# Kernel tuning notes

Hardware: AMD Instinct MI355X
Metric: run time of the kernel (lower is better)

The kernel has to match this reference:

```python
import jax, jax.numpy as jnp
import numpy as np

B, T, SDR, D, H = 2, 1024, 2048, 1024, 16
DH = D // H
FFN_H = int(D * 4.0 * 2 / 3)  # SwiGLU 2/3 rule -> 2730
N_FHN_STEPS = 4
FHN_DT = 0.1
FHN_A = 0.7
FHN_B = 0.8
FHN_TAU = 12.5
FHN_THRESHOLD = 0.5


def _layernorm(x, g, b, eps=1e-5):
    mu = jnp.mean(x, axis=-1, keepdims=True)
    var = jnp.var(x, axis=-1, keepdims=True)
    return (x - mu) * jax.lax.rsqrt(var + eps) * g + b


def setup_inputs() -> dict:
    key = jax.random.key(0)
    ks = jax.random.split(key, 16)
    s = 0.02
    return {
        "sdr": jax.random.normal(ks[0], (B, T, SDR), jnp.float32),
        "sdr_w": jax.random.normal(ks[1], (SDR, D), jnp.float32) * s,
        "sdr_b": jnp.zeros((D,), jnp.float32),
        "w_qkv": jax.random.normal(ks[2], (D, 3 * D), jnp.float32) * s,
        "b_qkv": jnp.zeros((3 * D,), jnp.float32),
        "w_out": jax.random.normal(ks[3], (D, D), jnp.float32) * s,
        "b_out": jnp.zeros((D,), jnp.float32),
        "ln1_g": jnp.ones((D,), jnp.float32),
        "ln1_b": jnp.zeros((D,), jnp.float32),
        "ln2_g": jnp.ones((D,), jnp.float32),
        "ln2_b": jnp.zeros((D,), jnp.float32),
        "w_gate": jax.random.normal(ks[4], (D, FFN_H), jnp.float32) * s,
        "w_up": jax.random.normal(ks[5], (D, FFN_H), jnp.float32) * s,
        "w_down": jax.random.normal(ks[6], (FFN_H, D), jnp.float32) * s,
    }


def _fhn_attention(h, w_qkv, b_qkv, w_out, b_out):
    # h: (B, T, D). Causal MHA whose pre-softmax scores are evolved by
    # FitzHugh-Nagumo soliton dynamics with IMEX (explicit v, implicit w) steps.
    qkv = h @ w_qkv + b_qkv
    q, k, vals = jnp.split(qkv, 3, axis=-1)
    q = q.reshape(B, T, H, DH).transpose(0, 2, 1, 3)      # bhtd
    k = k.reshape(B, T, H, DH).transpose(0, 2, 1, 3)
    vals = vals.reshape(B, T, H, DH).transpose(0, 2, 1, 3)
    scores = jnp.einsum("bhqd,bhkd->bhqk", q, k) / jnp.sqrt(jnp.float32(DH))
    # FHN IMEX integration: v' = v - v^3/3 - w + I ; tau w' = v + a - b w
    v = scores
    w = jnp.zeros_like(scores)
    w_denom = 1.0 + FHN_DT * FHN_B / FHN_TAU
    for _ in range(N_FHN_STEPS):
        v = v + FHN_DT * (v - v * v * v / 3.0 - w + scores)  # explicit
        w = (w + FHN_DT * (v + FHN_A) / FHN_TAU) / w_denom   # implicit linear
    logits = v - FHN_THRESHOLD
    causal = jnp.tril(jnp.ones((T, T), bool))
    logits = jnp.where(causal, logits, -1e9)
    attn = jax.nn.softmax(logits, axis=-1)
    ctx = jnp.einsum("bhqk,bhkd->bhqd", attn, vals)
    ctx = ctx.transpose(0, 2, 1, 3).reshape(B, T, D)
    return ctx @ w_out + b_out


def reference(sdr, sdr_w, sdr_b, w_qkv, b_qkv, w_out, b_out,
              ln1_g, ln1_b, ln2_g, ln2_b, w_gate, w_up, w_down):
    x = sdr @ sdr_w + sdr_b                                   # sdr_proj
    attn_out = _fhn_attention(_layernorm(x, ln1_g, ln1_b),
                              w_qkv, b_qkv, w_out, b_out)
    x = x + attn_out                                          # residual
    h2 = _layernorm(x, ln2_g, ln2_b)
    mlp = (jax.nn.silu(h2 @ w_gate) * (h2 @ w_up)) @ w_down   # SwiGLU
    return x + mlp
```

## Files before the change

kernel.cpp:

```cpp
#include <hip/hip_runtime.h>
#include <hip/hip_bf16.h>
#include <math.h>


typedef __bf16 bf16;
typedef __bf16 bf16x4 __attribute__((ext_vector_type(4)));
typedef __bf16 bf16x8 __attribute__((ext_vector_type(8)));
typedef float  f32x4  __attribute__((ext_vector_type(4)));

#define DEV __device__ __forceinline__

DEV void gload_lds16(const void* g, void* l) {
  __builtin_amdgcn_global_load_lds(
      (const __attribute__((address_space(1))) void*)g,
      (__attribute__((address_space(3))) void*)l, 16, 0, 0);
}

__global__ __launch_bounds__(256) void k_convert(const float* __restrict__ in,
                                                 bf16* __restrict__ out, int n) {
  int i = (blockIdx.x * 256 + threadIdx.x) * 4;
  if (i < n) {
    float4 f = *(const float4*)(in + i);
    bf16x4 o;
    o[0] = (bf16)f.x; o[1] = (bf16)f.y; o[2] = (bf16)f.z; o[3] = (bf16)f.w;
    *(bf16x4*)(out + i) = o;
  }
}

__global__ __launch_bounds__(256) void k_transpose_wt(const float* __restrict__ in,
    bf16* __restrict__ out, int K, int N, int Kpad, int Npad) {
  __shared__ float tile[32][33];
  const int kb = blockIdx.x * 32, nb = blockIdx.y * 32;
  const int tx = threadIdx.x & 31, ty = threadIdx.x >> 5;
  for (int i = ty; i < 32; i += 8) {
    int k = kb + i, n = nb + tx;
    tile[i][tx] = (k < K && n < N) ? in[(size_t)k * N + n] : 0.f;
  }
  __syncthreads();
  for (int i = ty; i < 32; i += 8) {
    int n = nb + i, k = kb + tx;
    if (n < Npad && k < Kpad) out[(size_t)n * Kpad + k] = (bf16)tile[tx][i];
  }
}

__global__ __launch_bounds__(256) void k_layernorm(const float* __restrict__ x,
    const float* __restrict__ gw, const float* __restrict__ bw, bf16* __restrict__ out) {
  const int row = blockIdx.x;
  const int t = threadIdx.x;
  const float* xr = x + (size_t)row * 1024;
  float4 f = *(const float4*)(xr + t * 4);
  float s  = f.x + f.y + f.z + f.w;
  float s2 = f.x * f.x + f.y * f.y + f.z * f.z + f.w * f.w;
  #pragma unroll
  for (int o = 32; o > 0; o >>= 1) { s += __shfl_down(s, o, 64); s2 += __shfl_down(s2, o, 64); }
  __shared__ float rA[4], rB[4];
  const int wid = t >> 6;
  if ((t & 63) == 0) { rA[wid] = s; rB[wid] = s2; }
  __syncthreads();
  s  = rA[0] + rA[1] + rA[2] + rA[3];
  s2 = rB[0] + rB[1] + rB[2] + rB[3];
  const float mu   = s * (1.f / 1024.f);
  const float var  = fmaxf(s2 * (1.f / 1024.f) - mu * mu, 0.f);
  const float rstd = rsqrtf(var + 1e-5f);
  float4 g4 = *(const float4*)(gw + t * 4);
  float4 b4 = *(const float4*)(bw + t * 4);
  bf16x4 o4;
  o4[0] = (bf16)((f.x - mu) * rstd * g4.x + b4.x);
  o4[1] = (bf16)((f.y - mu) * rstd * g4.y + b4.y);
  o4[2] = (bf16)((f.z - mu) * rstd * g4.z + b4.z);
  o4[3] = (bf16)((f.w - mu) * rstd * g4.w + b4.w);
  *(bf16x4*)(out + (size_t)row * 1024 + t * 4) = o4;
}

enum { EPI_BIAS = 1, EPI_BIAS_RES = 2, EPI_RES = 3, EPI_QKV = 5 };

template <int EPI>
DEV void gemm_epilogue(int rb, int cc, int Nn, const f32x4& a,
                       float* C, const float* bias, const float* res,
                       bf16* qp, bf16* kp, float* vbuf) {
  float bv = 0.f;
  if constexpr (EPI == EPI_BIAS || EPI == EPI_BIAS_RES || EPI == EPI_QKV) bv = bias[cc];
  #pragma unroll
  for (int v = 0; v < 4; ++v) {
    const int row = rb + v;
    float val = a[v] + bv;
    if constexpr (EPI == EPI_QKV) {
      const int bq = row >> 10, tt = row & 1023;
      if (cc < 1024) {
        qp[(size_t)(bq * 16 + (cc >> 6)) * 65536 + (size_t)tt * 64 + (cc & 63)] = (bf16)(val * 0.125f);
      } else if (cc < 2048) {
        const int c2 = cc - 1024;
        kp[(size_t)(bq * 16 + (c2 >> 6)) * 65536 + (size_t)tt * 64 + (c2 & 63)] = (bf16)val;
      } else {
        vbuf[(size_t)row * 1024 + (cc - 2048)] = val;
      }
    } else {
      const size_t idx = (size_t)row * Nn + cc;
      if constexpr (EPI == EPI_BIAS_RES || EPI == EPI_RES) val += res[idx];
      C[idx] = val;
    }
  }
}

template <int EPI>
__global__ __launch_bounds__(256, 2)
void k_gemm(const bf16* __restrict__ A, const bf16* __restrict__ Bt,
            float* __restrict__ C, const float* __restrict__ bias,
            const float* __restrict__ res, bf16* __restrict__ qp,
            bf16* __restrict__ kp, float* __restrict__ vbuf, int Nn, int Kk) {
  __shared__ __align__(16) bf16 As[128 * 64];
  __shared__ __align__(16) bf16 Bs[128 * 64];
  const int t = threadIdx.x;
  const int lane = t & 63, wid = t >> 6;
  const int wr = wid >> 1, wc = wid & 1;
  const int row0 = blockIdx.y * 128, col0 = blockIdx.x * 128;
  const int g  = t & 7;
  const int r0 = t >> 3;
  const int c16s = g ^ (r0 & 7);
  f32x4 acc[4][4] = {};

  for (int k0 = 0; k0 < Kk; k0 += 64) {
    #pragma unroll
    for (int it = 0; it < 4; ++it) {
      int r = r0 + it * 32;
      gload_lds16(A + (size_t)(row0 + r) * Kk + k0 + c16s * 8, &As[(it * 256 + wid * 64) * 8]);
    }
    #pragma unroll
    for (int it = 0; it < 4; ++it) {
      int r = r0 + it * 32;
      gload_lds16(Bt + (size_t)(col0 + r) * Kk + k0 + c16s * 8, &Bs[(it * 256 + wid * 64) * 8]);
    }
    __syncthreads();
    #pragma unroll
    for (int ks = 0; ks < 2; ++ks) {
      bf16x8 af[4], bfv[4];
      #pragma unroll
      for (int m = 0; m < 4; ++m) {
        int rr = wr * 64 + m * 16 + (lane & 15);
        int c16 = (ks * 4 + (lane >> 4)) ^ (rr & 7);
        af[m] = *(const bf16x8*)&As[rr * 64 + c16 * 8];
      }
      #pragma unroll
      for (int n = 0; n < 4; ++n) {
        int rr = wc * 64 + n * 16 + (lane & 15);
        int c16 = (ks * 4 + (lane >> 4)) ^ (rr & 7);
        bfv[n] = *(const bf16x8*)&Bs[rr * 64 + c16 * 8];
      }
      #pragma unroll
      for (int m = 0; m < 4; ++m)
        #pragma unroll
        for (int n = 0; n < 4; ++n)
          acc[m][n] = __builtin_amdgcn_mfma_f32_16x16x32_bf16(af[m], bfv[n], acc[m][n], 0, 0, 0);
    }
    __syncthreads();
  }
  #pragma unroll
  for (int m = 0; m < 4; ++m) {
    const int rb = row0 + wr * 64 + m * 16 + ((lane >> 4) << 2);
    #pragma unroll
    for (int n = 0; n < 4; ++n) {
      const int cc = col0 + wc * 64 + n * 16 + (lane & 15);
      gemm_epilogue<EPI>(rb, cc, Nn, acc[m][n], C, bias, res, qp, kp, vbuf);
    }
  }
}

template <int EPI>
__global__ __launch_bounds__(256, 2)
void k_gemm64(const bf16* __restrict__ A, const bf16* __restrict__ Bt,
              float* __restrict__ C, const float* __restrict__ bias,
              const float* __restrict__ res, int Nn, int Kk) {
  __shared__ __align__(16) bf16 As[128 * 64];
  __shared__ __align__(16) bf16 Bs[64 * 64];
  const int t = threadIdx.x;
  const int lane = t & 63, wid = t >> 6;
  const int row0 = blockIdx.y * 128, col0 = blockIdx.x * 64;
  const int g  = t & 7;
  const int r0 = t >> 3;
  const int c16s = g ^ (r0 & 7);
  f32x4 acc[2][4] = {};

  for (int k0 = 0; k0 < Kk; k0 += 64) {
    #pragma unroll
    for (int it = 0; it < 4; ++it) {
      int r = r0 + it * 32;
      gload_lds16(A + (size_t)(row0 + r) * Kk + k0 + c16s * 8, &As[(it * 256 + wid * 64) * 8]);
    }
    #pragma unroll
    for (int it = 0; it < 2; ++it) {
      int r = r0 + it * 32;
      gload_lds16(Bt + (size_t)(col0 + r) * Kk + k0 + c16s * 8, &Bs[(it * 256 + wid * 64) * 8]);
    }
    __syncthreads();
    #pragma unroll
    for (int ks = 0; ks < 2; ++ks) {
      bf16x8 af[2], bfv[4];
      #pragma unroll
      for (int m = 0; m < 2; ++m) {
        int rr = wid * 32 + m * 16 + (lane & 15);
        int c16 = (ks * 4 + (lane >> 4)) ^ (rr & 7);
        af[m] = *(const bf16x8*)&As[rr * 64 + c16 * 8];
      }
      #pragma unroll
      for (int n = 0; n < 4; ++n) {
        int rr = n * 16 + (lane & 15);
        int c16 = (ks * 4 + (lane >> 4)) ^ (rr & 7);
        bfv[n] = *(const bf16x8*)&Bs[rr * 64 + c16 * 8];
      }
      #pragma unroll
      for (int m = 0; m < 2; ++m)
        #pragma unroll
        for (int n = 0; n < 4; ++n)
          acc[m][n] = __builtin_amdgcn_mfma_f32_16x16x32_bf16(af[m], bfv[n], acc[m][n], 0, 0, 0);
    }
    __syncthreads();
  }
  #pragma unroll
  for (int m = 0; m < 2; ++m) {
    const int rb = row0 + wid * 32 + m * 16 + ((lane >> 4) << 2);
    #pragma unroll
    for (int n = 0; n < 4; ++n) {
      const int cc = col0 + n * 16 + (lane & 15);
      gemm_epilogue<EPI>(rb, cc, Nn, acc[m][n], C, bias, res, nullptr, nullptr, nullptr);
    }
  }
}

__global__ __launch_bounds__(256, 2)
void k_gemm_swiglu(const bf16* __restrict__ A, const bf16* __restrict__ Bg,
                   const bf16* __restrict__ Bu, bf16* __restrict__ act,
                   int Nn, int Kk) {
  __shared__ __align__(16) bf16 As[128 * 64];
  __shared__ __align__(16) bf16 Bgs[128 * 64];
  __shared__ __align__(16) bf16 Bus[128 * 64];
  const int t = threadIdx.x;
  const int lane = t & 63, wid = t >> 6;
  const int wr = wid >> 1, wc = wid & 1;
  const int row0 = blockIdx.y * 128, col0 = blockIdx.x * 128;
  const int g  = t & 7;
  const int r0 = t >> 3;
  const int c16s = g ^ (r0 & 7);
  f32x4 ag[4][4] = {}, au[4][4] = {};

  for (int k0 = 0; k0 < Kk; k0 += 64) {
    #pragma unroll
    for (int it = 0; it < 4; ++it) {
      int r = r0 + it * 32;
      gload_lds16(A + (size_t)(row0 + r) * Kk + k0 + c16s * 8, &As[(it * 256 + wid * 64) * 8]);
    }
    #pragma unroll
    for (int it = 0; it < 4; ++it) {
      int r = r0 + it * 32;
      gload_lds16(Bg + (size_t)(col0 + r) * Kk + k0 + c16s * 8, &Bgs[(it * 256 + wid * 64) * 8]);
    }
    #pragma unroll
    for (int it = 0; it < 4; ++it) {
      int r = r0 + it * 32;
      gload_lds16(Bu + (size_t)(col0 + r) * Kk + k0 + c16s * 8, &Bus[(it * 256 + wid * 64) * 8]);
    }
    __syncthreads();
    #pragma unroll
    for (int ks = 0; ks < 2; ++ks) {
      bf16x8 af[4], bg[4], bu[4];
      #pragma unroll
      for (int m = 0; m < 4; ++m) {
        int rr = wr * 64 + m * 16 + (lane & 15);
        int c16 = (ks * 4 + (lane >> 4)) ^ (rr & 7);
        af[m] = *(const bf16x8*)&As[rr * 64 + c16 * 8];
      }
      #pragma unroll
      for (int n = 0; n < 4; ++n) {
        int rr = wc * 64 + n * 16 + (lane & 15);
        int c16 = (ks * 4 + (lane >> 4)) ^ (rr & 7);
        bg[n] = *(const bf16x8*)&Bgs[rr * 64 + c16 * 8];
        bu[n] = *(const bf16x8*)&Bus[rr * 64 + c16 * 8];
      }
      #pragma unroll
      for (int m = 0; m < 4; ++m)
        #pragma unroll
        for (int n = 0; n < 4; ++n) {
          ag[m][n] = __builtin_amdgcn_mfma_f32_16x16x32_bf16(af[m], bg[n], ag[m][n], 0, 0, 0);
          au[m][n] = __builtin_amdgcn_mfma_f32_16x16x32_bf16(af[m], bu[n], au[m][n], 0, 0, 0);
        }
    }
    __syncthreads();
  }
  #pragma unroll
  for (int m = 0; m < 4; ++m) {
    const int rb = row0 + wr * 64 + m * 16 + ((lane >> 4) << 2);
    #pragma unroll
    for (int n = 0; n < 4; ++n) {
      const int cc = col0 + wc * 64 + n * 16 + (lane & 15);
      #pragma unroll
      for (int v = 0; v < 4; ++v) {
        float gt = ag[m][n][v], up = au[m][n][v];
        float sg = gt / (1.f + __expf(-gt));
        act[(size_t)(rb + v) * Nn + cc] = (bf16)(sg * up);
      }
    }
  }
}

__global__ __launch_bounds__(256) void k_transpose_v(const float* __restrict__ vbuf,
                                                     bf16* __restrict__ vT) {
  __shared__ float tile[32][33];
  const int bh = blockIdx.z, b = bh >> 4, h = bh & 15;
  const int t0 = blockIdx.x * 32, d0 = blockIdx.y * 32;
  const int tx = threadIdx.x & 31, ty = threadIdx.x >> 5;
  for (int i = ty; i < 32; i += 8)
    tile[i][tx] = vbuf[(size_t)(b * 1024 + t0 + i) * 1024 + h * 64 + d0 + tx];
  __syncthreads();
  for (int i = ty; i < 32; i += 8)
    vT[(size_t)bh * 65536 + (size_t)(d0 + i) * 1024 + t0 + tx] = (bf16)tile[tx][i];
}

#define FHN_DT 0.1f
#define FHN_A_ 0.7f

__global__ __launch_bounds__(256, 4)
void k_attn(const bf16* __restrict__ q, const bf16* __restrict__ k,
            const bf16* __restrict__ vT, bf16* __restrict__ ctx) {
  __shared__ __align__(16) char smem[16896];
  const int bx = blockIdx.x;
  const int s  = 63 - (bx >> 5);
  const int bh = bx & 31;
  const int b = bh >> 4, hh = bh & 15;
  const int t = threadIdx.x;
  const int lane = t & 63, wid = t >> 6;
  const int l15 = lane & 15, g4 = lane >> 4;
  const int q0 = s * 16;
  bf16* Ps    = (bf16*)smem + wid * 1024;
  float* comb = (float*)smem;
  float* mlb  = (float*)(smem + 16384);
  const bf16* qb = q  + (size_t)bh * 65536;
  const bf16* kb = k  + (size_t)bh * 65536;
  const bf16* vb = vT + (size_t)bh * 65536;
  const float wden = 1.0f / (1.0f + FHN_DT * 0.8f / 12.5f);
  const float dtau = FHN_DT / 12.5f;

  bf16x8 qf[2];
  #pragma unroll
  for (int ks = 0; ks < 2; ++ks)
    qf[ks] = *(const bf16x8*)(qb + (size_t)(q0 + l15) * 64 + ks * 32 + g4 * 8);

  f32x4 o[4] = {};
  f32x4 mrow = {-1e30f, -1e30f, -1e30f, -1e30f};
  f32x4 ssum = {0.f, 0.f, 0.f, 0.f};
  const int jn = (q0 >> 6) + 1;

  for (int j = wid; j < jn; j += 4) {
    const int kv0 = j * 64;
    f32x4 sc[4] = {};
    #pragma unroll
    for (int ks = 0; ks < 2; ++ks)
      #pragma unroll
      for (int n = 0; n < 4; ++n) {
        bf16x8 kf = *(const bf16x8*)(kb + (size_t)(kv0 + n * 16 + l15) * 64 + ks * 32 + g4 * 8);
        sc[n] = __builtin_amdgcn_mfma_f32_16x16x32_bf16(qf[ks], kf, sc[n], 0, 0, 0);
      }
    const int rbase = q0 + (g4 << 2);
    #pragma unroll
    for (int n = 0; n < 4; ++n)
      #pragma unroll
      for (int v = 0; v < 4; ++v) {
        float sv = sc[n][v];
        float vv = sv, ww = 0.f;
        #pragma unroll
        for (int st = 0; st < 4; ++st) {
          vv = vv + FHN_DT * (vv - vv * vv * vv * (1.f / 3.f) - ww + sv);
          ww = (ww + dtau * (vv + FHN_A_)) * wden;
        }
        float lg = vv - 0.5f;
        if (j == jn - 1) {
          int kvi = kv0 + n * 16 + l15;
          if (kvi > rbase + v) lg = -1e9f;
        }
        sc[n][v] = lg;
      }
    f32x4 mnew, scl;
    #pragma unroll
    for (int v = 0; v < 4; ++v) {
      float m0 = fmaxf(fmaxf(sc[0][v], sc[1][v]), fmaxf(sc[2][v], sc[3][v]));
      #pragma unroll
      for (int msk = 1; msk < 16; msk <<= 1) m0 = fmaxf(m0, __shfl_xor(m0, msk, 64));
      mnew[v] = fmaxf(mrow[v], m0);
      scl[v] = __expf(mrow[v] - mnew[v]);
    }
    #pragma unroll
    for (int v = 0; v < 4; ++v) {
      float rs = 0.f;
      #pragma unroll
      for (int n = 0; n < 4; ++n) {
        float p = __expf(sc[n][v] - mnew[v]);
        sc[n][v] = p;
        rs += p;
      }
      #pragma unroll
      for (int msk = 1; msk < 16; msk <<= 1) rs += __shfl_xor(rs, msk, 64);
      ssum[v] = ssum[v] * scl[v] + rs;
      mrow[v] = mnew[v];
    }
    #pragma unroll
    for (int n = 0; n < 4; ++n) o[n] *= scl;
    #pragma unroll
    for (int n = 0; n < 4; ++n)
      #pragma unroll
      for (int v = 0; v < 4; ++v) {
        int rr = (g4 << 2) + v;
        int c = n * 16 + l15;
        int c16 = (c >> 3) ^ (rr & 7);
        Ps[rr * 64 + c16 * 8 + (c & 7)] = (bf16)sc[n][v];
      }
    #pragma unroll
    for (int ks = 0; ks < 2; ++ks) {
      int c16 = (ks * 4 + g4) ^ (l15 & 7);
      bf16x8 pa = *(const bf16x8*)&Ps[l15 * 64 + c16 * 8];
      #pragma unroll
      for (int n = 0; n < 4; ++n) {
        bf16x8 vf = *(const bf16x8*)(vb + (size_t)(n * 16 + l15) * 1024 + kv0 + ks * 32 + g4 * 8);
        o[n] = __builtin_amdgcn_mfma_f32_16x16x32_bf16(pa, vf, o[n], 0, 0, 0);
      }
    }
  }
  __syncthreads();
  #pragma unroll
  for (int n = 0; n < 4; ++n)
    #pragma unroll
    for (int v = 0; v < 4; ++v)
      comb[(wid * 16 + (g4 << 2) + v) * 64 + n * 16 + l15] = o[n][v];
  if (l15 == 0) {
    #pragma unroll
    for (int v = 0; v < 4; ++v) {
      mlb[(wid * 16 + (g4 << 2) + v) * 2 + 0] = mrow[v];
      mlb[(wid * 16 + (g4 << 2) + v) * 2 + 1] = ssum[v];
    }
  }
  __syncthreads();
  {
    const int row = t >> 4, dseg = t & 15;
    float m = mlb[row * 2];
    #pragma unroll
    for (int w = 1; w < 4; ++w) m = fmaxf(m, mlb[(w * 16 + row) * 2]);
    float L = 0.f;
    f32x4 a = {0.f, 0.f, 0.f, 0.f};
    #pragma unroll
    for (int w = 0; w < 4; ++w) {
      float f = __expf(mlb[(w * 16 + row) * 2] - m);
      L += f * mlb[(w * 16 + row) * 2 + 1];
      f32x4 c = *(const f32x4*)&comb[(w * 16 + row) * 64 + dseg * 4];
      a += c * f;
    }
    const float inv = 1.f / L;
    bf16x4 o4;
    o4[0] = (bf16)(a[0] * inv); o4[1] = (bf16)(a[1] * inv);
    o4[2] = (bf16)(a[2] * inv); o4[3] = (bf16)(a[3] * inv);
    *(bf16x4*)&ctx[(size_t)(b * 1024 + q0 + row) * 1024 + hh * 64 + dseg * 4] = o4;
  }
}

extern "C" void kernel_launch(void* const* d_in, const int* in_sizes, int n_in,
                              void* d_out, int out_size, void* d_ws, size_t ws_size,
                              hipStream_t stream) {
  (void)in_sizes; (void)n_in; (void)out_size; (void)ws_size;
  const float* sdr    = (const float*)d_in[0];
  const float* sdr_w  = (const float*)d_in[1];
  const float* sdr_b  = (const float*)d_in[2];
  const float* w_qkv  = (const float*)d_in[3];
  const float* b_qkv  = (const float*)d_in[4];
  const float* w_out  = (const float*)d_in[5];
  const float* b_out  = (const float*)d_in[6];
  const float* ln1_g  = (const float*)d_in[7];
  const float* ln1_b  = (const float*)d_in[8];
  const float* ln2_g  = (const float*)d_in[9];
  const float* ln2_b  = (const float*)d_in[10];
  const float* w_gate = (const float*)d_in[11];
  const float* w_up   = (const float*)d_in[12];
  const float* w_down = (const float*)d_in[13];
  float* out = (float*)d_out;

  char* wsb = (char*)d_ws;
  size_t off = 0;
  auto alloc = [&](size_t bytes) -> void* {
    void* p = (void*)(wsb + off);
    off += (bytes + 255) & ~(size_t)255;
    return p;
  };
  bf16* sdr_w_t  = (bf16*)alloc(1024ull * 2048 * 2);
  bf16* w_qkv_t  = (bf16*)alloc(3072ull * 1024 * 2);
  bf16* w_out_t  = (bf16*)alloc(1024ull * 1024 * 2);
  bf16* w_gate_t = (bf16*)alloc(2816ull * 1024 * 2);
  bf16* w_up_t   = (bf16*)alloc(2816ull * 1024 * 2);
  bf16* w_down_t = (bf16*)alloc(1024ull * 2816 * 2);
  bf16* big_bf   = (bf16*)alloc(2048ull * 2816 * 2);
  bf16* sdr_bf   = big_bf;
  bf16* act      = big_bf;
  float* x       = (float*)alloc(2048ull * 1024 * 4);
  bf16*  h       = (bf16*)alloc(2048ull * 1024 * 2);
  float* vbuf    = (float*)alloc(2048ull * 1024 * 4);
  bf16*  qb      = (bf16*)alloc(32ull * 1024 * 64 * 2);
  bf16*  kb      = (bf16*)alloc(32ull * 1024 * 64 * 2);
  bf16*  vT      = (bf16*)alloc(32ull * 1024 * 64 * 2);
  bf16*  ctx     = (bf16*)alloc(2048ull * 1024 * 2);
  float* x2      = (float*)alloc(2048ull * 1024 * 4);

  k_convert<<<4096, 256, 0, stream>>>(sdr, sdr_bf, 4194304);
  k_transpose_wt<<<dim3(64, 32),  256, 0, stream>>>(sdr_w,  sdr_w_t,  2048, 1024, 2048, 1024);
  k_transpose_wt<<<dim3(32, 96),  256, 0, stream>>>(w_qkv,  w_qkv_t,  1024, 3072, 1024, 3072);
  k_transpose_wt<<<dim3(32, 32),  256, 0, stream>>>(w_out,  w_out_t,  1024, 1024, 1024, 1024);
  k_transpose_wt<<<dim3(32, 88),  256, 0, stream>>>(w_gate, w_gate_t, 1024, 2730, 1024, 2816);
  k_transpose_wt<<<dim3(32, 88),  256, 0, stream>>>(w_up,   w_up_t,   1024, 2730, 1024, 2816);
  k_transpose_wt<<<dim3(88, 32),  256, 0, stream>>>(w_down, w_down_t, 2730, 1024, 2816, 1024);

  k_gemm64<EPI_BIAS><<<dim3(16, 16), 256, 0, stream>>>(sdr_bf, sdr_w_t, x, sdr_b, nullptr, 1024, 2048);
  k_layernorm<<<2048, 256, 0, stream>>>(x, ln1_g, ln1_b, h);
  k_gemm<EPI_QKV><<<dim3(24, 16), 256, 0, stream>>>(h, w_qkv_t, nullptr, b_qkv, nullptr, qb, kb, vbuf, 3072, 1024);
  k_transpose_v<<<dim3(32, 2, 32), 256, 0, stream>>>(vbuf, vT);
  k_attn<<<2048, 256, 0, stream>>>(qb, kb, vT, ctx);
  k_gemm64<EPI_BIAS_RES><<<dim3(16, 16), 256, 0, stream>>>(ctx, w_out_t, x2, b_out, x, 1024, 1024);
  k_layernorm<<<2048, 256, 0, stream>>>(x2, ln2_g, ln2_b, h);
  k_gemm_swiglu<<<dim3(22, 16), 256, 0, stream>>>(h, w_gate_t, w_up_t, act, 2816, 1024);
  k_gemm64<EPI_RES><<<dim3(16, 16), 256, 0, stream>>>(act, w_down_t, out, nullptr, x2, 1024, 2816);
}
```

Measured before the change: 356.6 us.

## Double-buffer GEMM LDS tiles and pair causal attention query blocks per workgroup

The k_gemm and k_gemm64 kernels now keep two LDS buffers, so the next K-slice's global-to-LDS loads are issued before the MFMA work on the current slice. This is meant to hide load latency, and it doubles the shared memory used per block, which may lower occupancy. The attention kernel now runs two query tiles per block, a long one (63-pr) and a short one (pr), and launches half as many blocks. This balances the causal workload across blocks and cuts scheduling overhead.

```diff
diff --git a/kernel.cpp b/kernel.cpp
--- a/kernel.cpp
+++ b/kernel.cpp
@@ -108,8 +108,8 @@
             float* __restrict__ C, const float* __restrict__ bias,
             const float* __restrict__ res, bf16* __restrict__ qp,
             bf16* __restrict__ kp, float* __restrict__ vbuf, int Nn, int Kk) {
-  __shared__ __align__(16) bf16 As[128 * 64];
-  __shared__ __align__(16) bf16 Bs[128 * 64];
+  __shared__ __align__(16) bf16 As[2][128 * 64];
+  __shared__ __align__(16) bf16 Bs[2][128 * 64];
   const int t = threadIdx.x;
   const int lane = t & 63, wid = t >> 6;
   const int wr = wid >> 1, wc = wid & 1;
@@ -119,18 +119,24 @@
   const int c16s = g ^ (r0 & 7);
   f32x4 acc[4][4] = {};
 
+  auto stage = [&](int buf, int k0) {
+    #pragma unroll
+    for (int it = 0; it < 4; ++it) {
+      int r = r0 + it * 32;
+      gload_lds16(A + (size_t)(row0 + r) * Kk + k0 + c16s * 8, &As[buf][(it * 256 + wid * 64) * 8]);
+    }
+    #pragma unroll
+    for (int it = 0; it < 4; ++it) {
+      int r = r0 + it * 32;
+      gload_lds16(Bt + (size_t)(col0 + r) * Kk + k0 + c16s * 8, &Bs[buf][(it * 256 + wid * 64) * 8]);
+    }
+  };
+
+  stage(0, 0);
+  __syncthreads();
+  int cur = 0;
   for (int k0 = 0; k0 < Kk; k0 += 64) {
-    #pragma unroll
-    for (int it = 0; it < 4; ++it) {
-      int r = r0 + it * 32;
-      gload_lds16(A + (size_t)(row0 + r) * Kk + k0 + c16s * 8, &As[(it * 256 + wid * 64) * 8]);
-    }
-    #pragma unroll
-    for (int it = 0; it < 4; ++it) {
-      int r = r0 + it * 32;
-      gload_lds16(Bt + (size_t)(col0 + r) * Kk + k0 + c16s * 8, &Bs[(it * 256 + wid * 64) * 8]);
-    }
-    __syncthreads();
+    if (k0 + 64 < Kk) stage(cur ^ 1, k0 + 64);
     #pragma unroll
     for (int ks = 0; ks < 2; ++ks) {
       bf16x8 af[4], bfv[4];
@@ -138,13 +144,13 @@
       for (int m = 0; m < 4; ++m) {
         int rr = wr * 64 + m * 16 + (lane & 15);
         int c16 = (ks * 4 + (lane >> 4)) ^ (rr & 7);
-        af[m] = *(const bf16x8*)&As[rr * 64 + c16 * 8];
+        af[m] = *(const bf16x8*)&As[cur][rr * 64 + c16 * 8];
       }
       #pragma unroll
       for (int n = 0; n < 4; ++n) {
         int rr = wc * 64 + n * 16 + (lane & 15);
         int c16 = (ks * 4 + (lane >> 4)) ^ (rr & 7);
-        bfv[n] = *(const bf16x8*)&Bs[rr * 64 + c16 * 8];
+        bfv[n] = *(const bf16x8*)&Bs[cur][rr * 64 + c16 * 8];
       }
       #pragma unroll
       for (int m = 0; m < 4; ++m)
@@ -153,6 +159,7 @@
           acc[m][n] = __builtin_amdgcn_mfma_f32_16x16x32_bf16(af[m], bfv[n], acc[m][n], 0, 0, 0);
     }
     __syncthreads();
+    cur ^= 1;
   }
   #pragma unroll
   for (int m = 0; m < 4; ++m) {
@@ -170,8 +177,8 @@
 void k_gemm64(const bf16* __restrict__ A, const bf16* __restrict__ Bt,
               float* __restrict__ C, const float* __restrict__ bias,
               const float* __restrict__ res, int Nn, int Kk) {
-  __shared__ __align__(16) bf16 As[128 * 64];
-  __shared__ __align__(16) bf16 Bs[64 * 64];
+  __shared__ __align__(16) bf16 As[2][128 * 64];
+  __shared__ __align__(16) bf16 Bs[2][64 * 64];
   const int t = threadIdx.x;
   const int lane = t & 63, wid = t >> 6;
   const int row0 = blockIdx.y * 128, col0 = blockIdx.x * 64;
@@ -180,18 +187,24 @@
   const int c16s = g ^ (r0 & 7);
   f32x4 acc[2][4] = {};
 
+  auto stage = [&](int buf, int k0) {
+    #pragma unroll
+    for (int it = 0; it < 4; ++it) {
+      int r = r0 + it * 32;
+      gload_lds16(A + (size_t)(row0 + r) * Kk + k0 + c16s * 8, &As[buf][(it * 256 + wid * 64) * 8]);
+    }
+    #pragma unroll
+    for (int it = 0; it < 2; ++it) {
+      int r = r0 + it * 32;
+      gload_lds16(Bt + (size_t)(col0 + r) * Kk + k0 + c16s * 8, &Bs[buf][(it * 256 + wid * 64) * 8]);
+    }
+  };
+
+  stage(0, 0);
+  __syncthreads();
+  int cur = 0;
   for (int k0 = 0; k0 < Kk; k0 += 64) {
-    #pragma unroll
-    for (int it = 0; it < 4; ++it) {
-      int r = r0 + it * 32;
-      gload_lds16(A + (size_t)(row0 + r) * Kk + k0 + c16s * 8, &As[(it * 256 + wid * 64) * 8]);
-    }
-    #pragma unroll
-    for (int it = 0; it < 2; ++it) {
-      int r = r0 + it * 32;
-      gload_lds16(Bt + (size_t)(col0 + r) * Kk + k0 + c16s * 8, &Bs[(it * 256 + wid * 64) * 8]);
-    }
-    __syncthreads();
+    if (k0 + 64 < Kk) stage(cur ^ 1, k0 + 64);
     #pragma unroll
     for (int ks = 0; ks < 2; ++ks) {
       bf16x8 af[2], bfv[4];
@@ -199,13 +212,13 @@
       for (int m = 0; m < 2; ++m) {
         int rr = wid * 32 + m * 16 + (lane & 15);
         int c16 = (ks * 4 + (lane >> 4)) ^ (rr & 7);
-        af[m] = *(const bf16x8*)&As[rr * 64 + c16 * 8];
+        af[m] = *(const bf16x8*)&As[cur][rr * 64 + c16 * 8];
       }
       #pragma unroll
       for (int n = 0; n < 4; ++n) {
         int rr = n * 16 + (lane & 15);
         int c16 = (ks * 4 + (lane >> 4)) ^ (rr & 7);
-        bfv[n] = *(const bf16x8*)&Bs[rr * 64 + c16 * 8];
+        bfv[n] = *(const bf16x8*)&Bs[cur][rr * 64 + c16 * 8];
       }
       #pragma unroll
       for (int m = 0; m < 2; ++m)
@@ -214,6 +227,7 @@
           acc[m][n] = __builtin_amdgcn_mfma_f32_16x16x32_bf16(af[m], bfv[n], acc[m][n], 0, 0, 0);
     }
     __syncthreads();
+    cur ^= 1;
   }
   #pragma unroll
   for (int m = 0; m < 2; ++m) {
@@ -322,13 +336,12 @@
             const bf16* __restrict__ vT, bf16* __restrict__ ctx) {
   __shared__ __align__(16) char smem[16896];
   const int bx = blockIdx.x;
-  const int s  = 63 - (bx >> 5);
+  const int pr = bx >> 5;
   const int bh = bx & 31;
   const int b = bh >> 4, hh = bh & 15;
   const int t = threadIdx.x;
   const int lane = t & 63, wid = t >> 6;
   const int l15 = lane & 15, g4 = lane >> 4;
-  const int q0 = s * 16;
   bf16* Ps    = (bf16*)smem + wid * 1024;
   float* comb = (float*)smem;
   float* mlb  = (float*)(smem + 16384);
@@ -338,123 +351,129 @@
   const float wden = 1.0f / (1.0f + FHN_DT * 0.8f / 12.5f);
   const float dtau = FHN_DT / 12.5f;
 
-  bf16x8 qf[2];
-  #pragma unroll
-  for (int ks = 0; ks < 2; ++ks)
-    qf[ks] = *(const bf16x8*)(qb + (size_t)(q0 + l15) * 64 + ks * 32 + g4 * 8);
-
-  f32x4 o[4] = {};
-  f32x4 mrow = {-1e30f, -1e30f, -1e30f, -1e30f};
-  f32x4 ssum = {0.f, 0.f, 0.f, 0.f};
-  const int jn = (q0 >> 6) + 1;
-
-  for (int j = wid; j < jn; j += 4) {
-    const int kv0 = j * 64;
-    f32x4 sc[4] = {};
+  #pragma unroll 1
+  for (int ph = 0; ph < 2; ++ph) {
+    const int s  = ph ? pr : 63 - pr;
+    const int q0 = s * 16;
+    bf16x8 qf[2];
     #pragma unroll
     for (int ks = 0; ks < 2; ++ks)
-      #pragma unroll
-      for (int n = 0; n < 4; ++n) {
-        bf16x8 kf = *(const bf16x8*)(kb + (size_t)(kv0 + n * 16 + l15) * 64 + ks * 32 + g4 * 8);
-        sc[n] = __builtin_amdgcn_mfma_f32_16x16x32_bf16(qf[ks], kf, sc[n], 0, 0, 0);
-      }
-    const int rbase = q0 + (g4 << 2);
+      qf[ks] = *(const bf16x8*)(qb + (size_t)(q0 + l15) * 64 + ks * 32 + g4 * 8);
+
+    f32x4 o[4] = {};
+    f32x4 mrow = {-1e30f, -1e30f, -1e30f, -1e30f};
+    f32x4 ssum = {0.f, 0.f, 0.f, 0.f};
+    const int jn = (q0 >> 6) + 1;
+
+    for (int j = wid; j < jn; j += 4) {
+      const int kv0 = j * 64;
+      f32x4 sc[4] = {};
+      #pragma unroll
+      for (int ks = 0; ks < 2; ++ks)
+        #pragma unroll
+        for (int n = 0; n < 4; ++n) {
+          bf16x8 kf = *(const bf16x8*)(kb + (size_t)(kv0 + n * 16 + l15) * 64 + ks * 32 + g4 * 8);
+          sc[n] = __builtin_amdgcn_mfma_f32_16x16x32_bf16(qf[ks], kf, sc[n], 0, 0, 0);
+        }
+      const int rbase = q0 + (g4 << 2);
+      #pragma unroll
+      for (int n = 0; n < 4; ++n)
+        #pragma unroll
+        for (int v = 0; v < 4; ++v) {
+          float sv = sc[n][v];
+          float vv = sv, ww = 0.f;
+          #pragma unroll
+          for (int st = 0; st < 4; ++st) {
+            vv = vv + FHN_DT * (vv - vv * vv * vv * (1.f / 3.f) - ww + sv);
+            ww = (ww + dtau * (vv + FHN_A_)) * wden;
+          }
+          float lg = vv - 0.5f;
+          if (j == jn - 1) {
+            int kvi = kv0 + n * 16 + l15;
+            if (kvi > rbase + v) lg = -1e9f;
+          }
+          sc[n][v] = lg;
+        }
+      f32x4 mnew, scl;
+      #pragma unroll
+      for (int v = 0; v < 4; ++v) {
+        float m0 = fmaxf(fmaxf(sc[0][v], sc[1][v]), fmaxf(sc[2][v], sc[3][v]));
+        #pragma unroll
+        for (int msk = 1; msk < 16; msk <<= 1) m0 = fmaxf(m0, __shfl_xor(m0, msk, 64));
+        mnew[v] = fmaxf(mrow[v], m0);
+        scl[v] = __expf(mrow[v] - mnew[v]);
+      }
+      #pragma unroll
+      for (int v = 0; v < 4; ++v) {
+        float rs = 0.f;
+        #pragma unroll
+        for (int n = 0; n < 4; ++n) {
+          float p = __expf(sc[n][v] - mnew[v]);
+          sc[n][v] = p;
+          rs += p;
+        }
+        #pragma unroll
+        for (int msk = 1; msk < 16; msk <<= 1) rs += __shfl_xor(rs, msk, 64);
+        ssum[v] = ssum[v] * scl[v] + rs;
+        mrow[v] = mnew[v];
+      }
+      #pragma unroll
+      for (int n = 0; n < 4; ++n) o[n] *= scl;
+      #pragma unroll
+      for (int n = 0; n < 4; ++n)
+        #pragma unroll
+        for (int v = 0; v < 4; ++v) {
+          int rr = (g4 << 2) + v;
+          int c = n * 16 + l15;
+          int c16 = (c >> 3) ^ (rr & 7);
+          Ps[rr * 64 + c16 * 8 + (c & 7)] = (bf16)sc[n][v];
+        }
+      #pragma unroll
+      for (int ks = 0; ks < 2; ++ks) {
+        int c16 = (ks * 4 + g4) ^ (l15 & 7);
+        bf16x8 pa = *(const bf16x8*)&Ps[l15 * 64 + c16 * 8];
+        #pragma unroll
+        for (int n = 0; n < 4; ++n) {
+          bf16x8 vf = *(const bf16x8*)(vb + (size_t)(n * 16 + l15) * 1024 + kv0 + ks * 32 + g4 * 8);
+          o[n] = __builtin_amdgcn_mfma_f32_16x16x32_bf16(pa, vf, o[n], 0, 0, 0);
+        }
+      }
+    }
+    __syncthreads();
     #pragma unroll
     for (int n = 0; n < 4; ++n)
       #pragma unroll
+      for (int v = 0; v < 4; ++v)
+        comb[(wid * 16 + (g4 << 2) + v) * 64 + n * 16 + l15] = o[n][v];
+    if (l15 == 0) {
+      #pragma unroll
       for (int v = 0; v < 4; ++v) {
-        float sv = sc[n][v];
-        float vv = sv, ww = 0.f;
-        #pragma unroll
-        for (int st = 0; st < 4; ++st) {
-          vv = vv + FHN_DT * (vv - vv * vv * vv * (1.f / 3.f) - ww + sv);
-          ww = (ww + dtau * (vv + FHN_A_)) * wden;
-        }
-        float lg = vv - 0.5f;
-        if (j == jn - 1) {
-          int kvi = kv0 + n * 16 + l15;
-          if (kvi > rbase + v) lg = -1e9f;
-        }
-        sc[n][v] = lg;
-      }
-    f32x4 mnew, scl;
-    #pragma unroll
-    for (int v = 0; v < 4; ++v) {
-      float m0 = fmaxf(fmaxf(sc[0][v], sc[1][v]), fmaxf(sc[2][v], sc[3][v]));
-      #pragma unroll
-      for (int msk = 1; msk < 16; msk <<= 1) m0 = fmaxf(m0, __shfl_xor(m0, msk, 64));
-      mnew[v] = fmaxf(mrow[v], m0);
-      scl[v] = __expf(mrow[v] - mnew[v]);
-    }
-    #pragma unroll
-    for (int v = 0; v < 4; ++v) {
-      float rs = 0.f;
-      #pragma unroll
-      for (int n = 0; n < 4; ++n) {
-        float p = __expf(sc[n][v] - mnew[v]);
-        sc[n][v] = p;
-        rs += p;
-      }
-      #pragma unroll
-      for (int msk = 1; msk < 16; msk <<= 1) rs += __shfl_xor(rs, msk, 64);
-      ssum[v] = ssum[v] * scl[v] + rs;
-      mrow[v] = mnew[v];
-    }
-    #pragma unroll
-    for (int n = 0; n < 4; ++n) o[n] *= scl;
-    #pragma unroll
-    for (int n = 0; n < 4; ++n)
-      #pragma unroll
-      for (int v = 0; v < 4; ++v) {
-        int rr = (g4 << 2) + v;
-        int c = n * 16 + l15;
-        int c16 = (c >> 3) ^ (rr & 7);
-        Ps[rr * 64 + c16 * 8 + (c & 7)] = (bf16)sc[n][v];
-      }
-    #pragma unroll
-    for (int ks = 0; ks < 2; ++ks) {
-      int c16 = (ks * 4 + g4) ^ (l15 & 7);
-      bf16x8 pa = *(const bf16x8*)&Ps[l15 * 64 + c16 * 8];
-      #pragma unroll
-      for (int n = 0; n < 4; ++n) {
-        bf16x8 vf = *(const bf16x8*)(vb + (size_t)(n * 16 + l15) * 1024 + kv0 + ks * 32 + g4 * 8);
-        o[n] = __builtin_amdgcn_mfma_f32_16x16x32_bf16(pa, vf, o[n], 0, 0, 0);
-      }
-    }
-  }
-  __syncthreads();
-  #pragma unroll
-  for (int n = 0; n < 4; ++n)
-    #pragma unroll
-    for (int v = 0; v < 4; ++v)
-      comb[(wid * 16 + (g4 << 2) + v) * 64 + n * 16 + l15] = o[n][v];
-  if (l15 == 0) {
-    #pragma unroll
-    for (int v = 0; v < 4; ++v) {
-      mlb[(wid * 16 + (g4 << 2) + v) * 2 + 0] = mrow[v];
-      mlb[(wid * 16 + (g4 << 2) + v) * 2 + 1] = ssum[v];
-    }
-  }
-  __syncthreads();
-  {
-    const int row = t >> 4, dseg = t & 15;
-    float m = mlb[row * 2];
-    #pragma unroll
-    for (int w = 1; w < 4; ++w) m = fmaxf(m, mlb[(w * 16 + row) * 2]);
-    float L = 0.f;
-    f32x4 a = {0.f, 0.f, 0.f, 0.f};
-    #pragma unroll
-    for (int w = 0; w < 4; ++w) {
-      float f = __expf(mlb[(w * 16 + row) * 2] - m);
-      L += f * mlb[(w * 16 + row) * 2 + 1];
-      f32x4 c = *(const f32x4*)&comb[(w * 16 + row) * 64 + dseg * 4];
-      a += c * f;
-    }
-    const float inv = 1.f / L;
-    bf16x4 o4;
-    o4[0] = (bf16)(a[0] * inv); o4[1] = (bf16)(a[1] * inv);
-    o4[2] = (bf16)(a[2] * inv); o4[3] = (bf16)(a[3] * inv);
-    *(bf16x4*)&ctx[(size_t)(b * 1024 + q0 + row) * 1024 + hh * 64 + dseg * 4] = o4;
+        mlb[(wid * 16 + (g4 << 2) + v) * 2 + 0] = mrow[v];
+        mlb[(wid * 16 + (g4 << 2) + v) * 2 + 1] = ssum[v];
+      }
+    }
+    __syncthreads();
+    {
+      const int row = t >> 4, dseg = t & 15;
+      float m = mlb[row * 2];
+      #pragma unroll
+      for (int w = 1; w < 4; ++w) m = fmaxf(m, mlb[(w * 16 + row) * 2]);
+      float L = 0.f;
+      f32x4 a = {0.f, 0.f, 0.f, 0.f};
+      #pragma unroll
+      for (int w = 0; w < 4; ++w) {
+        float f = __expf(mlb[(w * 16 + row) * 2] - m);
+        L += f * mlb[(w * 16 + row) * 2 + 1];
+        f32x4 c = *(const f32x4*)&comb[(w * 16 + row) * 64 + dseg * 4];
+        a += c * f;
+      }
+      const float inv = 1.f / L;
+      bf16x4 o4;
+      o4[0] = (bf16)(a[0] * inv); o4[1] = (bf16)(a[1] * inv);
+      o4[2] = (bf16)(a[2] * inv); o4[3] = (bf16)(a[3] * inv);
+      *(bf16x4*)&ctx[(size_t)(b * 1024 + q0 + row) * 1024 + hh * 64 + dseg * 4] = o4;
+    }
+    __syncthreads();
   }
 }
 
@@ -515,7 +534,7 @@
   k_layernorm<<<2048, 256, 0, stream>>>(x, ln1_g, ln1_b, h);
   k_gemm<EPI_QKV><<<dim3(24, 16), 256, 0, stream>>>(h, w_qkv_t, nullptr, b_qkv, nullptr, qb, kb, vbuf, 3072, 1024);
   k_transpose_v<<<dim3(32, 2, 32), 256, 0, stream>>>(vbuf, vT);
-  k_attn<<<2048, 256, 0, stream>>>(qb, kb, vT, ctx);
+  k_attn<<<1024, 256, 0, stream>>>(qb, kb, vT, ctx);
   k_gemm64<EPI_BIAS_RES><<<dim3(16, 16), 256, 0, stream>>>(ctx, w_out_t, x2, b_out, x, 1024, 1024);
   k_layernorm<<<2048, 256, 0, stream>>>(x2, ln2_g, ln2_b, h);
   k_gemm_swiglu<<<dim3(22, 16), 256, 0, stream>>>(h, w_gate_t, w_up_t, act, 2816, 1024);
```

Result: slower. 366.2 us (+2.7%).
